# Kernel tuning notes

Hardware: AMD Instinct MI355X
Metric: run time of the kernel (lower is better)

Reference implementation:

```python
import jax, jax.numpy as jnp
import numpy as np

EPS = 1e-4          # ReEig epsilon buffer
IN_SIZE = 4096      # input SPD matrix is IN_SIZE x IN_SIZE
HID = 5             # hard-coded bottleneck in RiemSPD
OUT_SIZE = 2048     # output SPD matrix is OUT_SIZE x OUT_SIZE


def _orthogonal(key, rows, cols):
    # mimic nn.init.orthogonal_: semi-orthogonal (rows, cols) matrix
    n, m = max(rows, cols), min(rows, cols)
    a = jax.random.normal(key, (n, m), dtype=jnp.float32)
    q, _ = jnp.linalg.qr(a)
    q = q[:, :m]
    return q if rows >= cols else q.T


def bimap(x, w):
    # BiMap.forward: W^T @ X @ W
    return w.T @ (x @ w)


def rectify(x):
    # Rectify.forward: SVD, clip singular values at EPS, rebuild u diag(s) u^T
    u, s, _ = jnp.linalg.svd(x)
    s = jnp.maximum(s, EPS)
    return (u * s[None, :]) @ u.T


def setup_inputs() -> dict:
    key = jax.random.key(0)
    k1, k2, k3 = jax.random.split(key, 3)
    X = jax.random.normal(k1, (1, IN_SIZE, IN_SIZE), dtype=jnp.float32)
    W1 = _orthogonal(k2, IN_SIZE, HID)   # encoder BiMap weight (in_size, 5)
    W2 = _orthogonal(k3, HID, OUT_SIZE)  # decoder BiMap weight (5, out_size)
    return {"X": X, "W1": W1, "W2": W2}


def reference(X, W1, W2):
    x = X[0]                       # squeeze(0): (IN_SIZE, IN_SIZE)
    y = rectify(bimap(x, W1))      # encoder: (5, 5)
    z = rectify(bimap(y, W2))      # decoder: (OUT_SIZE, OUT_SIZE)
    return z
```

## Files before the change

kernel.cpp:

```cpp
#include <hip/hip_runtime.h>
#include <math.h>

static constexpr int N   = 4096;
static constexpr int H   = 5;
static constexpr int NO  = 2048;
static constexpr float FEPS = 1e-4f;
static constexpr int RPB  = 8;
static constexpr int NBLK = N / RPB;

#if __has_builtin(__builtin_amdgcn_rcpf)
__device__ __forceinline__ float frcp(float x) { return __builtin_amdgcn_rcpf(x); }
#else
__device__ __forceinline__ float frcp(float x) { return 1.0f / x; }
#endif
#if __has_builtin(__builtin_amdgcn_rsqf)
__device__ __forceinline__ float frsq(float x) { return __builtin_amdgcn_rsqf(x); }
#else
__device__ __forceinline__ float frsq(float x) { return 1.0f / sqrtf(x); }
#endif

__device__ __forceinline__ float wave_reduce(float v) {
#pragma unroll
    for (int o = 32; o > 0; o >>= 1) v += __shfl_down(v, o, 64);
    return v;
}

__global__ __launch_bounds__(256) void k_xw1(const float* __restrict__ X,
                                             const float* __restrict__ W1,
                                             float* __restrict__ Mp) {
    const int rb = blockIdx.x * RPB;
    const int t  = threadIdx.x;
    const float4* W14 = reinterpret_cast<const float4*>(W1);

    float acc[RPB][H];
#pragma unroll
    for (int r = 0; r < RPB; ++r)
#pragma unroll
        for (int a = 0; a < H; ++a) acc[r][a] = 0.f;

#pragma unroll
    for (int c = 0; c < 4; ++c) {
        const int j4 = c * 256 + t;
        float wf[20];
        {
            const float4 f0 = W14[5 * j4 + 0];
            const float4 f1 = W14[5 * j4 + 1];
            const float4 f2 = W14[5 * j4 + 2];
            const float4 f3 = W14[5 * j4 + 3];
            const float4 f4 = W14[5 * j4 + 4];
            wf[0]=f0.x;  wf[1]=f0.y;  wf[2]=f0.z;  wf[3]=f0.w;
            wf[4]=f1.x;  wf[5]=f1.y;  wf[6]=f1.z;  wf[7]=f1.w;
            wf[8]=f2.x;  wf[9]=f2.y;  wf[10]=f2.z; wf[11]=f2.w;
            wf[12]=f3.x; wf[13]=f3.y; wf[14]=f3.z; wf[15]=f3.w;
            wf[16]=f4.x; wf[17]=f4.y; wf[18]=f4.z; wf[19]=f4.w;
        }
#pragma unroll
        for (int r = 0; r < RPB; ++r) {
            const float4 x = reinterpret_cast<const float4*>(
                                 X + (size_t)(rb + r) * N)[j4];
#pragma unroll
            for (int a = 0; a < H; ++a)
                acc[r][a] += x.x * wf[a]      + x.y * wf[5 + a]
                           + x.z * wf[10 + a] + x.w * wf[15 + a];
        }
    }

    float m[H][H];
#pragma unroll
    for (int a = 0; a < H; ++a)
#pragma unroll
        for (int b = 0; b < H; ++b) m[a][b] = 0.f;
#pragma unroll
    for (int r = 0; r < RPB; ++r) {
        float w1r[H];
#pragma unroll
        for (int a = 0; a < H; ++a) w1r[a] = W1[(size_t)(rb + r) * H + a];
#pragma unroll
        for (int a = 0; a < H; ++a)
#pragma unroll
            for (int b = 0; b < H; ++b) m[a][b] += w1r[a] * acc[r][b];
    }

    __shared__ float sm[4][25];
    const int lane = t & 63, wv = t >> 6;
#pragma unroll
    for (int a = 0; a < H; ++a)
#pragma unroll
        for (int b = 0; b < H; ++b) {
            const float v = wave_reduce(m[a][b]);
            if (lane == 0) sm[wv][a * H + b] = v;
        }
    __syncthreads();
    if (t < 25)
        Mp[blockIdx.x * 25 + t] = sm[0][t] + sm[1][t] + sm[2][t] + sm[3][t];
}

#define JROT(p, q)                                                            \
    {                                                                         \
        const float apq = __shfl(a, (p) * 5 + (q), 64);                       \
        const float app = __shfl(a, (p) * 5 + (p), 64);                       \
        const float aqq = __shfl(a, (q) * 5 + (q), 64);                       \
        const bool  skip =                                                    \
            (apq * apq) <= (1e-26f * (app * app + aqq * aqq) + 1e-38f);       \
        const float theta = (aqq - app) * frcp(2.0f * apq);                   \
        const float tden  = fabsf(theta) + sqrtf(theta * theta + 1.0f);       \
        const float ttv   = ((theta >= 0.0f) ? 1.0f : -1.0f) * frcp(tden);    \
        float cc = frsq(ttv * ttv + 1.0f);                                    \
        float ss = ttv * cc;                                                  \
        cc = skip ? 1.0f : cc;                                                \
        ss = skip ? 0.0f : ss;                                                \
                                        \
        {                                                                     \
            const int  pr   = ((r == (p)) ? (q) : ((r == (q)) ? (p) : r));    \
            const float prt = __shfl(a, pr * 5 + c, 64);                      \
            a = (r == (p)) ? (cc * a - ss * prt)                              \
                           : ((r == (q)) ? (ss * prt + cc * a) : a);          \
        }                                                                     \
                                          \
        {                                                                     \
            const int  pc   = ((c == (p)) ? (q) : ((c == (q)) ? (p) : c));    \
            const float prt = __shfl(a, r * 5 + pc, 64);                      \
            a = (c == (p)) ? (cc * a - ss * prt)                              \
                           : ((c == (q)) ? (ss * prt + cc * a) : a);          \
            const float urt = __shfl(u, r * 5 + pc, 64);                      \
            u = (c == (p)) ? (cc * u - ss * urt)                              \
                           : ((c == (q)) ? (ss * urt + cc * u) : u);          \
        }                                                                     \
    }

__global__ __launch_bounds__(256) void k_small(const float* __restrict__ Mp,
                                               float* __restrict__ yp) {
    __shared__ float sred[10][26];
    __shared__ float Msum[25];
    const int t = threadIdx.x;

    if (t < 250) {
        const int e = t % 25, g = t / 25;
        float s = 0.f;
#pragma unroll 4
        for (int p = g; p < NBLK; p += 10) s += Mp[p * 25 + e];
        sred[g][e] = s;
    }
    __syncthreads();
    if (t < 25) {
        float s = 0.f;
#pragma unroll
        for (int g = 0; g < 10; ++g) s += sred[g][t];
        Msum[t] = s;
    }
    __syncthreads();

    if (t < 64) {
        const int r = t / 5, c = t % 5;
        const float m = (t < 25) ? Msum[t] : 0.f;

        float a = 0.f;
#pragma unroll
        for (int k = 0; k < H; ++k)
            a += __shfl(m, r * 5 + k, 64) * __shfl(m, c * 5 + k, 64);
        float u = (t < 25 && r == c) ? 1.0f : 0.0f;

        for (int sweep = 0; sweep < 6; ++sweep) {
            JROT(0, 1) JROT(0, 2) JROT(0, 3) JROT(0, 4) JROT(1, 2)
            JROT(1, 3) JROT(1, 4) JROT(2, 3) JROT(2, 4) JROT(3, 4)
        }

        const float ev = fmaxf(sqrtf(fmaxf(a, 0.0f)), FEPS);
        float yv = 0.f;
#pragma unroll
        for (int k = 0; k < H; ++k) {
            const float evk = __shfl(ev, 6 * k, 64);
            const float urk = __shfl(u, r * 5 + k, 64);
            const float uck = __shfl(u, c * 5 + k, 64);
            yv += evk * urk * uck;
        }
        if (t < 25) yp[t] = yv - ((r == c) ? FEPS : 0.f);
    }
}

__global__ __launch_bounds__(256) void k_out(const float* __restrict__ W2,
                                             const float* __restrict__ yp,
                                             float* __restrict__ Z) {
    const int i = blockIdx.x;
    const int t = threadIdx.x;

    float wcol[H];
#pragma unroll
    for (int k = 0; k < H; ++k) wcol[k] = W2[(size_t)k * NO + i];
    float c[H];
#pragma unroll
    for (int m = 0; m < H; ++m) {
        float s = 0.f;
#pragma unroll
        for (int k = 0; k < H; ++k) s += wcol[k] * yp[k * H + m];
        c[m] = s;
    }

#pragma unroll
    for (int hh = 0; hh < 2; ++hh) {
        const int jj = (hh * 256 + t) * 4;
        float zx = 0.f, zy = 0.f, zz = 0.f, zw = 0.f;
#pragma unroll
        for (int m = 0; m < H; ++m) {
            const float4 b = *reinterpret_cast<const float4*>(W2 + (size_t)m * NO + jj);
            zx += c[m] * b.x;
            zy += c[m] * b.y;
            zz += c[m] * b.z;
            zw += c[m] * b.w;
        }
        zx += (i == jj + 0) ? FEPS : 0.f;
        zy += (i == jj + 1) ? FEPS : 0.f;
        zz += (i == jj + 2) ? FEPS : 0.f;
        zw += (i == jj + 3) ? FEPS : 0.f;
        float4 o = make_float4(zx, zy, zz, zw);
        *reinterpret_cast<float4*>(Z + (size_t)i * NO + jj) = o;
    }
}

extern "C" void kernel_launch(void* const* d_in, const int* in_sizes, int n_in,
                              void* d_out, int out_size, void* d_ws, size_t ws_size,
                              hipStream_t stream) {
    const float* X  = (const float*)d_in[0];
    const float* W1 = (const float*)d_in[1];
    const float* W2 = (const float*)d_in[2];
    float* out = (float*)d_out;
    float* ws  = (float*)d_ws;

    float* Mp = ws;
    float* yp = ws + NBLK * 25;

    hipLaunchKernelGGL(k_xw1,   dim3(NBLK), dim3(256), 0, stream, X, W1, Mp);
    hipLaunchKernelGGL(k_small, dim3(1),    dim3(256), 0, stream, Mp, yp);
    hipLaunchKernelGGL(k_out,   dim3(NO),   dim3(256), 0, stream, W2, yp, out);
}
```

Before: 48.39 us.

## Fuse 5x5 eigen stage into output kernel and compute 8 output rows per block

Removes the single-block k_small launch. Each of the NO/8 output blocks now redundantly reduces the partial 5x5 sums and runs the Jacobi eigen-solve itself before writing its rows. Each block also computes 8 output rows, so the W2 column loads are reused across rows. This saves one kernel launch and the serial single-block stage, at the cost of repeating the small reduction and Jacobi work in 256 blocks.

```diff
diff --git a/kernel.cpp b/kernel.cpp
--- a/kernel.cpp
+++ b/kernel.cpp
@@ -7,6 +7,7 @@
 static constexpr float FEPS = 1e-4f;
 static constexpr int RPB  = 8;
 static constexpr int NBLK = N / RPB;
+static constexpr int NR   = 8;
 
 #if __has_builtin(__builtin_amdgcn_rcpf)
 __device__ __forceinline__ float frcp(float x) { return __builtin_amdgcn_rcpf(x); }
@@ -109,14 +110,12 @@
         float ss = ttv * cc;                                                  \
         cc = skip ? 1.0f : cc;                                                \
         ss = skip ? 0.0f : ss;                                                \
-                                        \
         {                                                                     \
             const int  pr   = ((r == (p)) ? (q) : ((r == (q)) ? (p) : r));    \
             const float prt = __shfl(a, pr * 5 + c, 64);                      \
             a = (r == (p)) ? (cc * a - ss * prt)                              \
                            : ((r == (q)) ? (ss * prt + cc * a) : a);          \
         }                                                                     \
-                                          \
         {                                                                     \
             const int  pc   = ((c == (p)) ? (q) : ((c == (q)) ? (p) : c));    \
             const float prt = __shfl(a, r * 5 + pc, 64);                      \
@@ -128,16 +127,18 @@
         }                                                                     \
     }
 
-__global__ __launch_bounds__(256) void k_small(const float* __restrict__ Mp,
-                                               float* __restrict__ yp) {
+__global__ __launch_bounds__(256) void k_out(const float* __restrict__ Mp,
+                                             const float* __restrict__ W2,
+                                             float* __restrict__ Z) {
     __shared__ float sred[10][26];
     __shared__ float Msum[25];
+    __shared__ float ys[25];
     const int t = threadIdx.x;
 
     if (t < 250) {
         const int e = t % 25, g = t / 25;
         float s = 0.f;
-#pragma unroll 4
+#pragma unroll 8
         for (int p = g; p < NBLK; p += 10) s += Mp[p * 25 + e];
         sred[g][e] = s;
     }
@@ -153,7 +154,6 @@
     if (t < 64) {
         const int r = t / 5, c = t % 5;
         const float m = (t < 25) ? Msum[t] : 0.f;
-
         float a = 0.f;
 #pragma unroll
         for (int k = 0; k < H; ++k)
@@ -174,46 +174,54 @@
             const float uck = __shfl(u, c * 5 + k, 64);
             yv += evk * urk * uck;
         }
-        if (t < 25) yp[t] = yv - ((r == c) ? FEPS : 0.f);
-    }
-}
-
-__global__ __launch_bounds__(256) void k_out(const float* __restrict__ W2,
-                                             const float* __restrict__ yp,
-                                             float* __restrict__ Z) {
-    const int i = blockIdx.x;
-    const int t = threadIdx.x;
-
-    float wcol[H];
-#pragma unroll
-    for (int k = 0; k < H; ++k) wcol[k] = W2[(size_t)k * NO + i];
-    float c[H];
-#pragma unroll
-    for (int m = 0; m < H; ++m) {
-        float s = 0.f;
-#pragma unroll
-        for (int k = 0; k < H; ++k) s += wcol[k] * yp[k * H + m];
-        c[m] = s;
+        if (t < 25) ys[t] = yv - ((r == c) ? FEPS : 0.f);
+    }
+    __syncthreads();
+
+    const int i0 = blockIdx.x * NR;
+    float cmat[NR][H];
+#pragma unroll
+    for (int r = 0; r < NR; ++r) {
+        float wcol[H];
+#pragma unroll
+        for (int k = 0; k < H; ++k) wcol[k] = W2[(size_t)k * NO + i0 + r];
+#pragma unroll
+        for (int m = 0; m < H; ++m) {
+            float s = 0.f;
+#pragma unroll
+            for (int k = 0; k < H; ++k) s += wcol[k] * ys[k * H + m];
+            cmat[r][m] = s;
+        }
     }
 
 #pragma unroll
     for (int hh = 0; hh < 2; ++hh) {
         const int jj = (hh * 256 + t) * 4;
-        float zx = 0.f, zy = 0.f, zz = 0.f, zw = 0.f;
-#pragma unroll
-        for (int m = 0; m < H; ++m) {
-            const float4 b = *reinterpret_cast<const float4*>(W2 + (size_t)m * NO + jj);
-            zx += c[m] * b.x;
-            zy += c[m] * b.y;
-            zz += c[m] * b.z;
-            zw += c[m] * b.w;
-        }
-        zx += (i == jj + 0) ? FEPS : 0.f;
-        zy += (i == jj + 1) ? FEPS : 0.f;
-        zz += (i == jj + 2) ? FEPS : 0.f;
-        zw += (i == jj + 3) ? FEPS : 0.f;
-        float4 o = make_float4(zx, zy, zz, zw);
-        *reinterpret_cast<float4*>(Z + (size_t)i * NO + jj) = o;
+        float4 w2j[H];
+#pragma unroll
+        for (int m = 0; m < H; ++m)
+            w2j[m] = *reinterpret_cast<const float4*>(W2 + (size_t)m * NO + jj);
+#pragma unroll
+        for (int r = 0; r < NR; ++r) {
+            const int i = i0 + r;
+            float zx = 0.f, zy = 0.f, zz = 0.f, zw = 0.f;
+#pragma unroll
+            for (int m = 0; m < H; ++m) {
+                const float cm = cmat[r][m];
+                zx += cm * w2j[m].x;
+                zy += cm * w2j[m].y;
+                zz += cm * w2j[m].z;
+                zw += cm * w2j[m].w;
+            }
+            if (i >= jj && i < jj + 4) {
+                if      (i == jj + 0) zx += FEPS;
+                else if (i == jj + 1) zy += FEPS;
+                else if (i == jj + 2) zz += FEPS;
+                else                  zw += FEPS;
+            }
+            *reinterpret_cast<float4*>(Z + (size_t)i * NO + jj) =
+                make_float4(zx, zy, zz, zw);
+        }
     }
 }
 
@@ -227,9 +235,7 @@
     float* ws  = (float*)d_ws;
 
     float* Mp = ws;
-    float* yp = ws + NBLK * 25;
-
-    hipLaunchKernelGGL(k_xw1,   dim3(NBLK), dim3(256), 0, stream, X, W1, Mp);
-    hipLaunchKernelGGL(k_small, dim3(1),    dim3(256), 0, stream, Mp, yp);
-    hipLaunchKernelGGL(k_out,   dim3(NO),   dim3(256), 0, stream, W2, yp, out);
-}
+
+    hipLaunchKernelGGL(k_xw1, dim3(NBLK),    dim3(256), 0, stream, X, W1, Mp);
+    hipLaunchKernelGGL(k_out, dim3(NO / NR), dim3(256), 0, stream, Mp, W2, out);
+}
```

Result: faster. 43.95 us (-9.2%).
